# Performance work log

Hardware: AMD Instinct MI355X
Metric: run time of the kernel (lower is better)

## Reference

```python
import math
import jax, jax.numpy as jnp
import numpy as np

TEMPERATURE = 1.0
TARGET_VARIANCE = 2.0


def _l2_normalize(x, eps=1e-12):
    # matches F.normalize(dim=-1): x / max(||x||_2, eps)
    n = jnp.linalg.norm(x, axis=-1, keepdims=True)
    return x / jnp.maximum(n, eps)


def setup_inputs() -> dict:
    key = jax.random.key(0)
    k1, k2, k3 = jax.random.split(key, 3)
    B, L, D = 16, 2048, 512
    embs = jax.random.normal(k1, (B, L, D), dtype=jnp.float32)
    clip_embs = jax.random.normal(k2, (B, L, D), dtype=jnp.float32)
    mask = jax.random.randint(k3, (B, L), 0, 2, dtype=jnp.int32)
    return {"embs": embs, "clip_embs": clip_embs, "mask": mask}


def reference(embs, clip_embs, mask):
    B, L, D = embs.shape
    p = _l2_normalize(embs)
    q = _l2_normalize(clip_embs)

    # m_b = number of valid tokens per sample; original slices the first m rows
    m = jnp.sum(mask > 0, axis=-1)                      # [B]
    valid = jnp.arange(L)[None, :] < m[:, None]         # [B, L]
    colm = valid[:, None, :]                            # [B, 1, L] column mask

    # batched p @ q^T over the full padded length, masked afterwards
    logits = jnp.einsum('bid,bjd->bij', p, q) / TEMPERATURE  # [B, L, L]
    neg = jnp.finfo(logits.dtype).min
    logp = jax.nn.log_softmax(jnp.where(colm, logits, neg), axis=-1)

    # Gaussian distance weights: base_weight[i, j] = |i - j|
    idx = jnp.arange(L)
    dist = jnp.abs(idx[:, None] - idx[None, :]).astype(embs.dtype)  # [L, L]
    t_un = jnp.exp(-(dist ** 2) / (2.0 * TARGET_VARIANCE ** 2)) / TARGET_VARIANCE * math.sqrt(math.pi * 2.0)
    target = jax.nn.softmax(jnp.where(colm, t_un[None], neg), axis=-1)  # [B, L, L]

    # KL(target || softmax(logits)) = target * (log target - logp), summed over cols
    safe_t = jnp.where(colm, target, 1.0)
    kl = jnp.where(colm, target * (jnp.log(safe_t) - logp), 0.0)
    row_sum = jnp.sum(kl, axis=-1)                      # [B, L]

    # mean over the m valid rows, then mean over batch
    per_sample = jnp.sum(jnp.where(valid, row_sum, 0.0), axis=-1) / m.astype(embs.dtype)
    return jnp.sum(per_sample) / B
```

## Files before the change

### kernel.cpp

```cpp
#include <hip/hip_runtime.h>
#include <hip/hip_bf16.h>

#define BB 16
#define LL 2048
#define DD 512
#define BL (BB*LL)
#define RADIUS 15
#define CF 1.25331414f
#define NSL 6
#define NII 16

typedef __attribute__((ext_vector_type(8))) short short8_t;
typedef __attribute__((ext_vector_type(4))) float f32x4;
typedef __attribute__((ext_vector_type(2))) long long2_t;

static __device__ __forceinline__ unsigned short f2bf(float x){
  unsigned int u = __float_as_uint(x);
  return (unsigned short)((u + 0x7fffu + ((u >> 16) & 1u)) >> 16);
}

static __device__ __forceinline__ void gld_lds16(const void* g, void* l){
  __builtin_amdgcn_global_load_lds(
      (const __attribute__((address_space(1))) unsigned int*)g,
      (__attribute__((address_space(3))) unsigned int*)l, 16, 0, 0);
}

#if __has_builtin(__builtin_amdgcn_cvt_pk_fp8_f32)
static __device__ __forceinline__ long f2fp8x8(float4 x0, float4 x1){
  int w0 = __builtin_amdgcn_cvt_pk_fp8_f32(x0.x, x0.y, 0, false);
  w0     = __builtin_amdgcn_cvt_pk_fp8_f32(x0.z, x0.w, w0, true);
  int w1 = __builtin_amdgcn_cvt_pk_fp8_f32(x1.x, x1.y, 0, false);
  w1     = __builtin_amdgcn_cvt_pk_fp8_f32(x1.z, x1.w, w1, true);
  return ((long)(unsigned)w1 << 32) | (unsigned)w0;
}
#else
static __device__ __forceinline__ unsigned f2fp8_1(float xf){
  unsigned x = __float_as_uint(xf);
  unsigned s = (x >> 24) & 0x80u;
  unsigned ax = x & 0x7fffffffu;
  if (ax >= 0x43e80000u) return s | 0x7eu;
  if (ax <  0x3a800000u) return s;
  unsigned exp = ax >> 23;
  if (exp <= 120){
    unsigned man = (ax & 0x7fffffu) | 0x800000u;
    int rsh = 141 - (int)exp;
    unsigned keep = man >> rsh;
    unsigned rem  = man & ((1u << rsh) - 1u);
    unsigned half = 1u << (rsh - 1);
    keep += (rem > half || (rem == half && (keep & 1u)));
    return s | keep;
  }
  unsigned keep = ax >> 20;
  unsigned rem  = ax & 0xfffffu;
  keep += (rem > 0x80000u || (rem == 0x80000u && (keep & 1u)));
  int code = (int)keep - (120 << 3);
  if (code >= 0x7f) code = 0x7e;
  return s | (unsigned)code;
}
static __device__ __forceinline__ long f2fp8x8(float4 x0, float4 x1){
  unsigned long o = 0;
  o |= (unsigned long)f2fp8_1(x0.x);
  o |= (unsigned long)f2fp8_1(x0.y) << 8;
  o |= (unsigned long)f2fp8_1(x0.z) << 16;
  o |= (unsigned long)f2fp8_1(x0.w) << 24;
  o |= (unsigned long)f2fp8_1(x1.x) << 32;
  o |= (unsigned long)f2fp8_1(x1.y) << 40;
  o |= (unsigned long)f2fp8_1(x1.z) << 48;
  o |= (unsigned long)f2fp8_1(x1.w) << 56;
  return (long)o;
}
#endif


__global__ void mcount_kernel(const int* __restrict__ mask, int* __restrict__ mout){
  int b = blockIdx.x;
  int s = 0;
  for (int j = threadIdx.x; j < LL; j += 256) s += (mask[(size_t)b*LL + j] > 0) ? 1 : 0;
  __shared__ int sred[256];
  sred[threadIdx.x] = s; __syncthreads();
  for (int k = 128; k; k >>= 1){
    if (threadIdx.x < k) sred[threadIdx.x] += sred[threadIdx.x + k];
    __syncthreads();
  }
  if (threadIdx.x == 0) mout[b] = sred[0];
}

__global__ __launch_bounds__(256) void precvt(const float* __restrict__ embs,
                                              const float* __restrict__ clip,
                                              const int* __restrict__ mcnt,
                                              unsigned char* __restrict__ p8,
                                              unsigned char* __restrict__ q8){
  const int lane = threadIdx.x & 63;
  const int g    = lane >> 4;
  const int c    = lane & 15;
  const int base = blockIdx.x * 16 + (threadIdx.x >> 6) * 4;
  const int gw   = base + g;

  const float* src; unsigned char* dst; int r, b; bool isP;
  if (gw < BL){ isP = true;  b = gw >> 11; r = gw & 2047;
                src = embs + (size_t)gw * DD; dst = p8 + (size_t)b * LL * DD; }
  else        { isP = false; int g2 = gw - BL; b = g2 >> 11; r = g2 & 2047;
                src = clip + (size_t)g2 * DD; dst = q8 + (size_t)b * LL * DD; }
  const int M   = mcnt[b];
  const int RND = isP ? ((M + 127) & ~127) : ((M + 15) & ~15);
  if (r >= RND) return;

  float4 v[8];
  #pragma unroll
  for (int k = 0; k < 8; ++k) v[k] = *(const float4*)(src + c * 32 + k * 4);
  float ss = 0.f;
  #pragma unroll
  for (int k = 0; k < 8; ++k)
    ss += v[k].x*v[k].x + v[k].y*v[k].y + v[k].z*v[k].z + v[k].w*v[k].w;
  #pragma unroll
  for (int m = 1; m < 16; m <<= 1) ss += __shfl_xor(ss, m, 64);
  const float s = 1.0f / fmaxf(sqrtf(ss), 1e-12f);
  #pragma unroll
  for (int k = 0; k < 8; ++k){
    v[k].x *= s; v[k].y *= s; v[k].z *= s; v[k].w *= s;
  }
  const long o0 = f2fp8x8(v[0], v[1]);
  const long o1 = f2fp8x8(v[2], v[3]);
  const long o2 = f2fp8x8(v[4], v[5]);
  const long o3 = f2fp8x8(v[6], v[7]);
  const int xr = (r >> 2) & 3;
  long2_t lo, hi;
  switch (xr){
    case 0: lo = (long2_t){o0, o1}; hi = (long2_t){o2, o3}; break;
    case 1: lo = (long2_t){o1, o0}; hi = (long2_t){o3, o2}; break;
    case 2: lo = (long2_t){o2, o3}; hi = (long2_t){o0, o1}; break;
    default:lo = (long2_t){o3, o2}; hi = (long2_t){o1, o0}; break;
  }
  unsigned char* wb = dst + ((size_t)(c * LL + r) << 5);
  *(long2_t*)(wb)      = lo;
  *(long2_t*)(wb + 16) = hi;
}

__global__ __launch_bounds__(256, 4) void gram8(
    const unsigned char* __restrict__ p8, const unsigned char* __restrict__ q8,
    const int* __restrict__ mcnt, float* __restrict__ part )
{
  const int bid = blockIdx.x;
  const int xcd = bid & 7;
  const int b   = (xcd << 1) | ((bid >> 3) & 1);
  const int ii  = (bid >> 4) & (NII - 1);
  const int js  = bid >> 8;
  const int M   = mcnt[b];
  const int nIt = (M + 127) >> 7;
  if (ii >= nIt) return;

  __shared__ alignas(16) unsigned char bsm[3][8192];
  __shared__ float gt[RADIUS + 1];

  const int tid  = threadIdx.x;
  const int wave = tid >> 6;
  const int lane = tid & 63;
  const int col  = lane & 15;
  const int kg   = lane >> 4;
  const int kswz = (kg ^ (col >> 2)) << 3;

  if (tid <= RADIUS)
    gt[tid] = expm1f(CF * __expf(-(float)(tid * tid) * 0.125f));
  __syncthreads();

  const unsigned char* pb = p8 + (size_t)b * LL * DD;
  const unsigned char* qb = q8 + (size_t)b * LL * DD;
  const int njt = (M + 15) >> 4;
  const int S   = (njt > js) ? ((njt - js + NSL - 1) / NSL) : 0;
  if (S == 0) return;

  #define STAGE(BF, JT) do {                                                     \
    const int _j0 = (JT) << 4;                                                   \
    _Pragma("unroll")                                                            \
    for (int u = 0; u < 2; ++u){                                                 \
      const int _kb0 = (wave << 1) + (u << 3);                                   \
      gld_lds16(qb + ((size_t)((_kb0 + (lane >> 5)) * LL + _j0) << 5)            \
                   + ((lane & 31) << 4),                                         \
                (void*)&bsm[BF][_kb0 << 9]);                                     \
    }                                                                            \
  } while (0)

  const int iw = (ii << 7) + (wave << 5);

  long a0[16], a1[16];
  #pragma unroll
  for (int kb = 0; kb < 16; ++kb){
    a0[kb] = *(const long*)(pb + ((size_t)(kb * LL + iw      + col) << 5) + kswz);
    a1[kb] = *(const long*)(pb + ((size_t)(kb * LL + iw + 16 + col) << 5) + kswz);
  }
  #pragma unroll
  for (int kb = 0; kb < 16; ++kb){
    asm volatile("" : "+v"(a0[kb]));
    asm volatile("" : "+v"(a1[kb]));
  }

  float es0[4]={0,0,0,0}, ls0[4]={0,0,0,0}, bg0[4]={0,0,0,0};
  float es1[4]={0,0,0,0}, ls1[4]={0,0,0,0}, bg1[4]={0,0,0,0};

  STAGE(0, js);
  if (S > 1) STAGE(1, js + NSL);

  for (int s = 0; s < S; ++s){
    if (s + 1 < S) { asm volatile("s_waitcnt vmcnt(2)" ::: "memory"); }
    else           { asm volatile("s_waitcnt vmcnt(0)" ::: "memory"); }
    __builtin_amdgcn_s_barrier();
    __builtin_amdgcn_sched_barrier(0);
    if (s + 2 < S) STAGE((s + 2) % 3, js + NSL * (s + 2));

    const int j0 = (js + NSL * s) << 4;
    f32x4 c0 = {0.f,0.f,0.f,0.f}, c1 = {0.f,0.f,0.f,0.f};
    const unsigned char* lb = &bsm[s % 3][(col << 5) + kswz];
    __builtin_amdgcn_s_setprio(1);
    #pragma unroll
    for (int kb = 0; kb < 16; ++kb){
      long bf8 = *(const long*)(lb + (kb << 9));
      c0 = __builtin_amdgcn_mfma_f32_16x16x32_fp8_fp8(a0[kb], bf8, c0, 0, 0, 0);
      c1 = __builtin_amdgcn_mfma_f32_16x16x32_fp8_fp8(a1[kb], bf8, c1, 0, 0, 0);
    }
    __builtin_amdgcn_s_setprio(0);
    const int j = j0 + col;
    if (j < M){
      const int dt0 = j - iw - (kg << 2);
      #pragma unroll
      for (int r = 0; r < 4; ++r){
        float lg = c0[r];
        es0[r] += __expf(lg); ls0[r] += lg;
        int d = dt0 - r; int ad = d < 0 ? -d : d;
        if (ad <= RADIUS) bg0[r] += gt[ad] * lg;
        float lh = c1[r];
        es1[r] += __expf(lh); ls1[r] += lh;
        int d1 = dt0 - 16 - r; int ad1 = d1 < 0 ? -d1 : d1;
        if (ad1 <= RADIUS) bg1[r] += gt[ad1] * lh;
      }
    }
  }
  #undef STAGE

  #pragma unroll
  for (int m = 1; m < 16; m <<= 1){
    #pragma unroll
    for (int r = 0; r < 4; ++r){
      es0[r] += __shfl_xor(es0[r], m, 64); es1[r] += __shfl_xor(es1[r], m, 64);
      ls0[r] += __shfl_xor(ls0[r], m, 64); ls1[r] += __shfl_xor(ls1[r], m, 64);
      bg0[r] += __shfl_xor(bg0[r], m, 64); bg1[r] += __shfl_xor(bg1[r], m, 64);
    }
  }
  if (col == 0){
    #pragma unroll
    for (int r = 0; r < 4; ++r){
      int ia = iw + (kg << 2) + r;
      *(float4*)&part[(((size_t)b * LL + ia) * NSL + js) * 4] = make_float4(es0[r], ls0[r], bg0[r], 0.f);
      int ib = ia + 16;
      *(float4*)&part[(((size_t)b * LL + ib) * NSL + js) * 4] = make_float4(es1[r], ls1[r], bg1[r], 0.f);
    }
  }
}

__global__ __launch_bounds__(256) void finalize1(const float* __restrict__ part,
                                                 const int* __restrict__ mcnt,
                                                 float* __restrict__ psum){
  const int b = blockIdx.x;
  const int M = mcnt[b];
  __shared__ float e1s[16], tts[16], S1[16], TT[16], red[256];
  const int tid = threadIdx.x;
  if (tid < 16){
    float u  = CF * __expf(-(float)(tid * tid) * 0.125f);
    float eu = __expf(u);
    e1s[tid] = eu - 1.0f;
    tts[tid] = u * eu;
  }
  __syncthreads();
  if (tid == 0){
    float a = 0.f, c = 0.f;
    S1[0] = 0.f; TT[0] = 0.f;
    for (int d = 1; d <= RADIUS; ++d){ a += e1s[d]; c += tts[d]; S1[d] = a; TT[d] = c; }
  }
  __syncthreads();
  const float e10 = e1s[0], tt0 = tts[0];
  float acc = 0.f;
  for (int i = tid; i < M; i += 256){
    float es = 0.f, ls = 0.f, bg = 0.f;
    #pragma unroll
    for (int h = 0; h < NSL; ++h){
      float4 v = *(const float4*)&part[(((size_t)b * LL + i) * NSL + h) * 4];
      es += v.x; ls += v.y; bg += v.z;
    }
    int rl = i < RADIUS ? i : RADIUS;
    int rr = (M - 1 - i) < RADIUS ? (M - 1 - i) : RADIUS;
    float Zt = (float)M + e10 + S1[rl] + S1[rr];
    float U  = tt0 + TT[rl] + TT[rr];
    acc += (U - ls - bg) / Zt + logf(es) - logf(Zt);
  }
  red[tid] = acc; __syncthreads();
  for (int k = 128; k; k >>= 1){
    if (tid < k) red[tid] += red[tid + k];
    __syncthreads();
  }
  if (tid == 0) psum[b] = red[0] / (float)M;
}

__global__ void finalize2(const float* __restrict__ psum, float* __restrict__ out){
  if (threadIdx.x == 0){
    float a = 0.f;
    for (int b = 0; b < BB; ++b) a += psum[b];
    out[0] = a / (float)BB;
  }
}

#define TI 32
#define TJ 32
#define LSTR 520

__global__ void fb_qnorm(const float* __restrict__ clip, float* __restrict__ invq){
  int row = blockIdx.x;
  const float* p = clip + (size_t)row * DD;
  float4 v = *(const float4*)(p + (threadIdx.x << 2));
  float ss = v.x*v.x + v.y*v.y + v.z*v.z + v.w*v.w;
  for (int m = 32; m; m >>= 1) ss += __shfl_down(ss, m, 64);
  __shared__ float red[2];
  if ((threadIdx.x & 63) == 0) red[threadIdx.x >> 6] = ss;
  __syncthreads();
  if (threadIdx.x == 0)
    invq[row] = 1.0f / fmaxf(sqrtf(red[0] + red[1]), 1e-12f);
}

__global__ __launch_bounds__(256) void fb_main(
    const float* __restrict__ embs, const float* __restrict__ clip,
    const float* __restrict__ invq, const int* __restrict__ mcnt,
    float* __restrict__ row_sums)
{
  const int b  = blockIdx.y;
  const int M  = mcnt[b];
  const int i0 = blockIdx.x * TI;
  if (i0 >= M) return;
  __shared__ alignas(16) unsigned short qlds[TJ * LSTR];
  __shared__ float gtab[RADIUS + 1];
  __shared__ float partials[2][TI][3];
  const int tid  = threadIdx.x;
  const int wave = tid >> 6;
  const int lane = tid & 63;
  const int col  = lane & 15;
  const int kg   = lane >> 4;
  const int isub = wave >> 1;
  const int jsub = wave & 1;
  const int iw   = i0 + isub * 16;
  if (tid <= RADIUS)
    gtab[tid] = expm1f(CF * expf(-(float)(tid * tid) * 0.125f));
  const int arow = iw + col;
  const float* prow = embs + ((size_t)b * LL + arow) * DD;
  float ss = 0.f;
  for (int kb = 0; kb < 16; ++kb){
    float4 x0 = *(const float4*)(prow + kb * 32 + kg * 8);
    float4 x1 = *(const float4*)(prow + kb * 32 + kg * 8 + 4);
    ss += x0.x*x0.x + x0.y*x0.y + x0.z*x0.z + x0.w*x0.w
        + x1.x*x1.x + x1.y*x1.y + x1.z*x1.z + x1.w*x1.w;
  }
  ss += __shfl_xor(ss, 16, 64);
  ss += __shfl_xor(ss, 32, 64);
  const float sp = 1.0f / fmaxf(sqrtf(ss), 1e-12f);
  short8_t afrag[16];
  for (int kb = 0; kb < 16; ++kb){
    float4 x0 = *(const float4*)(prow + kb * 32 + kg * 8);
    float4 x1 = *(const float4*)(prow + kb * 32 + kg * 8 + 4);
    short8_t f;
    f[0]=(short)f2bf(x0.x*sp); f[1]=(short)f2bf(x0.y*sp);
    f[2]=(short)f2bf(x0.z*sp); f[3]=(short)f2bf(x0.w*sp);
    f[4]=(short)f2bf(x1.x*sp); f[5]=(short)f2bf(x1.y*sp);
    f[6]=(short)f2bf(x1.z*sp); f[7]=(short)f2bf(x1.w*sp);
    afrag[kb] = f;
  }
  float es[4]={0,0,0,0}, lsm[4]={0,0,0,0}, bg[4]={0,0,0,0};
  const int nj = (M + TJ - 1) / TJ;
  for (int jt = 0; jt < nj; ++jt){
    const int jb = jt * TJ;
    __syncthreads();
    {
      const float* qbase = clip + ((size_t)b * LL + jb) * DD;
      for (int u = 0; u < 16; ++u){
        int f  = u * 256 + tid;
        int r  = f >> 7, c4 = f & 127;
        int j  = jb + r;
        ushort4 wv = make_ushort4(0,0,0,0);
        if (j < M){
          float s = invq[b * LL + j];
          float4 x = *(const float4*)(qbase + ((size_t)r << 9) + (c4 << 2));
          wv = make_ushort4(f2bf(x.x*s), f2bf(x.y*s), f2bf(x.z*s), f2bf(x.w*s));
        }
        *reinterpret_cast<ushort4*>(&qlds[r * LSTR + (c4 << 2)]) = wv;
      }
    }
    __syncthreads();
    const int j0 = jb + jsub * 16;
    f32x4 acc = {0.f,0.f,0.f,0.f};
    const unsigned short* bbase = &qlds[(jsub * 16 + col) * LSTR + kg * 8];
    #pragma unroll
    for (int kb = 0; kb < 16; ++kb){
      short8_t bfrag = *reinterpret_cast<const short8_t*>(bbase + kb * 32);
      acc = __builtin_amdgcn_mfma_f32_16x16x32_bf16(afrag[kb], bfrag, acc, 0, 0, 0);
    }
    const int j = j0 + col;
    if (j < M){
      const int dt = j - iw - kg * 4;
      #pragma unroll
      for (int r = 0; r < 4; ++r){
        float lg = acc[r];
        es[r]  += expf(lg);
        lsm[r] += lg;
        int d = dt - r; int ad = d < 0 ? -d : d;
        if (ad <= RADIUS) bg[r] += gtab[ad] * lg;
      }
    }
  }
  #pragma unroll
  for (int m = 1; m < 16; m <<= 1){
    #pragma unroll
    for (int r = 0; r < 4; ++r){
      es[r]  += __shfl_xor(es[r],  m, 64);
      lsm[r] += __shfl_xor(lsm[r], m, 64);
      bg[r]  += __shfl_xor(bg[r],  m, 64);
    }
  }
  if (col == 0){
    #pragma unroll
    for (int r = 0; r < 4; ++r){
      int lrow = isub * 16 + kg * 4 + r;
      partials[jsub][lrow][0] = es[r];
      partials[jsub][lrow][1] = lsm[r];
      partials[jsub][lrow][2] = bg[r];
    }
  }
  __syncthreads();
  if (tid < TI){
    int i = i0 + tid;
    if (i < M){
      float esf = partials[0][tid][0] + partials[1][tid][0];
      float lsf = partials[0][tid][1] + partials[1][tid][1];
      float bgf = partials[0][tid][2] + partials[1][tid][2];
      int dlo = (-RADIUS < -i) ? -i : -RADIUS;
      int dhi = (RADIUS > M - 1 - i) ? (M - 1 - i) : RADIUS;
      float Zt = (float)M, U = 0.f;
      for (int d = dlo; d <= dhi; ++d){
        float uu = CF * expf(-(float)(d * d) * 0.125f);
        float eu = expf(uu);
        Zt += eu - 1.0f;
        U  += uu * eu;
      }
      row_sums[(size_t)b * LL + i] = (U - lsf - bgf) / Zt + logf(esf / Zt);
    }
  }
}

__global__ void fb_finalize(const float* __restrict__ row_sums,
                            const int* __restrict__ mcnt, float* __restrict__ out){
  __shared__ float red[256];
  float acc = 0.f;
  for (int b = 0; b < BB; ++b){
    int M = mcnt[b];
    float s = 0.f;
    for (int i = threadIdx.x; i < M; i += 256) s += row_sums[(size_t)b * LL + i];
    red[threadIdx.x] = s; __syncthreads();
    for (int k = 128; k; k >>= 1){
      if (threadIdx.x < k) red[threadIdx.x] += red[threadIdx.x + k];
      __syncthreads();
    }
    if (threadIdx.x == 0) acc += red[0] / (float)M;
    __syncthreads();
  }
  if (threadIdx.x == 0) out[0] = acc / (float)BB;
}


extern "C" void kernel_launch(void* const* d_in, const int* in_sizes, int n_in,
                              void* d_out, int out_size, void* d_ws, size_t ws_size,
                              hipStream_t stream) {
  const float* embs = (const float*)d_in[0];
  const float* clip = (const float*)d_in[1];
  const int*   mask = (const int*)d_in[2];
  float* out = (float*)d_out;

  const size_t REQ = (size_t)2 * BL * DD
                   + (size_t)BB * LL * NSL * 4 * sizeof(float)
                   + 64 * sizeof(float);
  if (ws_size >= REQ){
    unsigned char* p8 = (unsigned char*)d_ws;
    unsigned char* q8 = p8 + (size_t)BL * DD;
    float* part = (float*)(q8 + (size_t)BL * DD);
    float* psum = part + (size_t)BB * LL * NSL * 4;
    int*   mcnt = (int*)(psum + 16);

    mcount_kernel<<<dim3(BB), 256, 0, stream>>>(mask, mcnt);
    precvt<<<dim3(2 * BL / 16), 256, 0, stream>>>(embs, clip, mcnt, p8, q8);
    gram8<<<dim3(16 * NSL * NII), 256, 0, stream>>>(p8, q8, mcnt, part);
    finalize1<<<dim3(BB), 256, 0, stream>>>(part, mcnt, psum);
    finalize2<<<1, 64, 0, stream>>>(psum, out);
  } else {
    float* ws   = (float*)d_ws;
    float* invq = ws;
    int*   mcnt = (int*)(ws + BL);
    float* rows = ws + BL + 16;
    fb_qnorm<<<dim3(BL), 128, 0, stream>>>(clip, invq);
    mcount_kernel<<<dim3(BB), 256, 0, stream>>>(mask, mcnt);
    fb_main<<<dim3(LL / TI, BB), 256, 0, stream>>>(embs, clip, invq, mcnt, rows);
    fb_finalize<<<1, 256, 0, stream>>>(rows, mcnt, out);
  }
}
```

Before: 55.65 us.

## Widen gram tile to 32 columns with double-buffered LDS staging

Doubles the column tile per loop iteration from 16 to 32, so each LDS stage holds 16KB and feeds four MFMA chains. This reuses the register-resident A fragments twice as much per stage and halves the number of loop iterations and barriers. It switches from a three-stage to a two-stage LDS pipeline that waits for all loads each iteration. It also skips the band-weight math on tiles far from the diagonal and lowers the occupancy hint, which risks exposing load latency and adding register pressure.

```diff
diff --git a/kernel.cpp b/kernel.cpp
--- a/kernel.cpp
+++ b/kernel.cpp
@@ -102,7 +102,7 @@
   else        { isP = false; int g2 = gw - BL; b = g2 >> 11; r = g2 & 2047;
                 src = clip + (size_t)g2 * DD; dst = q8 + (size_t)b * LL * DD; }
   const int M   = mcnt[b];
-  const int RND = isP ? ((M + 127) & ~127) : ((M + 15) & ~15);
+  const int RND = isP ? ((M + 127) & ~127) : ((M + 31) & ~31);
   if (r >= RND) return;
 
   float4 v[8];
@@ -136,7 +136,7 @@
   *(long2_t*)(wb + 16) = hi;
 }
 
-__global__ __launch_bounds__(256, 4) void gram8(
+__global__ __launch_bounds__(256, 3) void gram10(
     const unsigned char* __restrict__ p8, const unsigned char* __restrict__ q8,
     const int* __restrict__ mcnt, float* __restrict__ part )
 {
@@ -149,7 +149,7 @@
   const int nIt = (M + 127) >> 7;
   if (ii >= nIt) return;
 
-  __shared__ alignas(16) unsigned char bsm[3][8192];
+  __shared__ alignas(16) unsigned char bsm[2][16384];
   __shared__ float gt[RADIUS + 1];
 
   const int tid  = threadIdx.x;
@@ -165,18 +165,17 @@
 
   const unsigned char* pb = p8 + (size_t)b * LL * DD;
   const unsigned char* qb = q8 + (size_t)b * LL * DD;
-  const int njt = (M + 15) >> 4;
+  const int njt = (M + 31) >> 5;
   const int S   = (njt > js) ? ((njt - js + NSL - 1) / NSL) : 0;
   if (S == 0) return;
 
   #define STAGE(BF, JT) do {                                                     \
-    const int _j0 = (JT) << 4;                                                   \
+    const int _j0 = (JT) << 5;                                                   \
     _Pragma("unroll")                                                            \
-    for (int u = 0; u < 2; ++u){                                                 \
-      const int _kb0 = (wave << 1) + (u << 3);                                   \
-      gld_lds16(qb + ((size_t)((_kb0 + (lane >> 5)) * LL + _j0) << 5)            \
-                   + ((lane & 31) << 4),                                         \
-                (void*)&bsm[BF][_kb0 << 9]);                                     \
+    for (int u = 0; u < 4; ++u){                                                 \
+      const int _kb = (wave << 2) + u;                                           \
+      gld_lds16(qb + ((size_t)(_kb * LL + _j0) << 5) + (lane << 4),              \
+                (void*)&bsm[BF][_kb << 10]);                                     \
     }                                                                            \
   } while (0)
 
@@ -188,51 +187,70 @@
     a0[kb] = *(const long*)(pb + ((size_t)(kb * LL + iw      + col) << 5) + kswz);
     a1[kb] = *(const long*)(pb + ((size_t)(kb * LL + iw + 16 + col) << 5) + kswz);
   }
-  #pragma unroll
-  for (int kb = 0; kb < 16; ++kb){
-    asm volatile("" : "+v"(a0[kb]));
-    asm volatile("" : "+v"(a1[kb]));
-  }
 
   float es0[4]={0,0,0,0}, ls0[4]={0,0,0,0}, bg0[4]={0,0,0,0};
   float es1[4]={0,0,0,0}, ls1[4]={0,0,0,0}, bg1[4]={0,0,0,0};
 
   STAGE(0, js);
-  if (S > 1) STAGE(1, js + NSL);
-
+  asm volatile("s_waitcnt vmcnt(0)" ::: "memory");
+  __builtin_amdgcn_s_barrier();
+  __builtin_amdgcn_sched_barrier(0);
+
+  int buf = 0;
   for (int s = 0; s < S; ++s){
-    if (s + 1 < S) { asm volatile("s_waitcnt vmcnt(2)" ::: "memory"); }
-    else           { asm volatile("s_waitcnt vmcnt(0)" ::: "memory"); }
+    if (s + 1 < S) STAGE(buf ^ 1, js + NSL * (s + 1));
+
+    const int j0 = (js + NSL * s) << 5;
+    f32x4 cA0 = {0.f,0.f,0.f,0.f}, cA1 = {0.f,0.f,0.f,0.f};
+    f32x4 cB0 = {0.f,0.f,0.f,0.f}, cB1 = {0.f,0.f,0.f,0.f};
+    const unsigned char* lb = &bsm[buf][(col << 5) + kswz];
+    #pragma unroll
+    for (int kb = 0; kb < 16; ++kb){
+      long bfA = *(const long*)(lb + (kb << 10));
+      long bfB = *(const long*)(lb + (kb << 10) + 512);
+      cA0 = __builtin_amdgcn_mfma_f32_16x16x32_fp8_fp8(a0[kb], bfA, cA0, 0, 0, 0);
+      cA1 = __builtin_amdgcn_mfma_f32_16x16x32_fp8_fp8(a1[kb], bfA, cA1, 0, 0, 0);
+      cB0 = __builtin_amdgcn_mfma_f32_16x16x32_fp8_fp8(a0[kb], bfB, cB0, 0, 0, 0);
+      cB1 = __builtin_amdgcn_mfma_f32_16x16x32_fp8_fp8(a1[kb], bfB, cB1, 0, 0, 0);
+    }
+    const int jA = j0 + col, jB = j0 + 16 + col;
+    const bool bandw = (j0 + 31 >= iw - RADIUS) && (j0 <= iw + 31 + RADIUS);
+    const int dtA = jA - iw - (kg << 2);
+    if (jA < M){
+      #pragma unroll
+      for (int r = 0; r < 4; ++r){
+        float lg = cA0[r];
+        float lh = cA1[r];
+        es0[r] += __expf(lg); ls0[r] += lg;
+        es1[r] += __expf(lh); ls1[r] += lh;
+        if (bandw){
+          int d = dtA - r; int ad = d < 0 ? -d : d;
+          if (ad <= RADIUS) bg0[r] += gt[ad] * lg;
+          int d1 = dtA - 16 - r; int ad1 = d1 < 0 ? -d1 : d1;
+          if (ad1 <= RADIUS) bg1[r] += gt[ad1] * lh;
+        }
+      }
+    }
+    if (jB < M){
+      const int dtB = dtA + 16;
+      #pragma unroll
+      for (int r = 0; r < 4; ++r){
+        float lg = cB0[r];
+        float lh = cB1[r];
+        es0[r] += __expf(lg); ls0[r] += lg;
+        es1[r] += __expf(lh); ls1[r] += lh;
+        if (bandw){
+          int d = dtB - r; int ad = d < 0 ? -d : d;
+          if (ad <= RADIUS) bg0[r] += gt[ad] * lg;
+          int d1 = dtB - 16 - r; int ad1 = d1 < 0 ? -d1 : d1;
+          if (ad1 <= RADIUS) bg1[r] += gt[ad1] * lh;
+        }
+      }
+    }
+    asm volatile("s_waitcnt vmcnt(0)" ::: "memory");
     __builtin_amdgcn_s_barrier();
     __builtin_amdgcn_sched_barrier(0);
-    if (s + 2 < S) STAGE((s + 2) % 3, js + NSL * (s + 2));
-
-    const int j0 = (js + NSL * s) << 4;
-    f32x4 c0 = {0.f,0.f,0.f,0.f}, c1 = {0.f,0.f,0.f,0.f};
-    const unsigned char* lb = &bsm[s % 3][(col << 5) + kswz];
-    __builtin_amdgcn_s_setprio(1);
-    #pragma unroll
-    for (int kb = 0; kb < 16; ++kb){
-      long bf8 = *(const long*)(lb + (kb << 9));
-      c0 = __builtin_amdgcn_mfma_f32_16x16x32_fp8_fp8(a0[kb], bf8, c0, 0, 0, 0);
-      c1 = __builtin_amdgcn_mfma_f32_16x16x32_fp8_fp8(a1[kb], bf8, c1, 0, 0, 0);
-    }
-    __builtin_amdgcn_s_setprio(0);
-    const int j = j0 + col;
-    if (j < M){
-      const int dt0 = j - iw - (kg << 2);
-      #pragma unroll
-      for (int r = 0; r < 4; ++r){
-        float lg = c0[r];
-        es0[r] += __expf(lg); ls0[r] += lg;
-        int d = dt0 - r; int ad = d < 0 ? -d : d;
-        if (ad <= RADIUS) bg0[r] += gt[ad] * lg;
-        float lh = c1[r];
-        es1[r] += __expf(lh); ls1[r] += lh;
-        int d1 = dt0 - 16 - r; int ad1 = d1 < 0 ? -d1 : d1;
-        if (ad1 <= RADIUS) bg1[r] += gt[ad1] * lh;
-      }
-    }
+    buf ^= 1;
   }
   #undef STAGE
 
@@ -490,7 +508,7 @@
 
     mcount_kernel<<<dim3(BB), 256, 0, stream>>>(mask, mcnt);
     precvt<<<dim3(2 * BL / 16), 256, 0, stream>>>(embs, clip, mcnt, p8, q8);
-    gram8<<<dim3(16 * NSL * NII), 256, 0, stream>>>(p8, q8, mcnt, part);
+    gram10<<<dim3(16 * NSL * NII), 256, 0, stream>>>(p8, q8, mcnt, part);
     finalize1<<<dim3(BB), 256, 0, stream>>>(part, mcnt, psum);
     finalize2<<<1, 64, 0, stream>>>(psum, out);
   } else {
```

After: 58.31 us. +4.8%, slower.

## Halve per-wave row tile in gram kernel and raise grid and occupancy

Applied to the files above, without the earlier changes.

The gram kernel now gives each wave 16 query rows (64 per block) instead of 32 (128 per block). It doubles the row-block count to 32, cuts the column slices from 6 to 5, and raises the launch bound to 6 blocks per CU. This lowers register pressure and adds parallelism and occupancy, but each staged key tile is reused by half as many MFMAs, so LDS and global traffic per FLOP rises. The setprio hints around the MFMA loop are also removed.

```diff
diff --git a/kernel.cpp b/kernel.cpp
--- a/kernel.cpp
+++ b/kernel.cpp
@@ -7,8 +7,8 @@
 #define BL (BB*LL)
 #define RADIUS 15
 #define CF 1.25331414f
-#define NSL 6
-#define NII 16
+#define NSL 5
+#define NII 32
 
 typedef __attribute__((ext_vector_type(8))) short short8_t;
 typedef __attribute__((ext_vector_type(4))) float f32x4;
@@ -136,7 +136,7 @@
   *(long2_t*)(wb + 16) = hi;
 }
 
-__global__ __launch_bounds__(256, 4) void gram8(
+__global__ __launch_bounds__(256, 6) void gram12(
     const unsigned char* __restrict__ p8, const unsigned char* __restrict__ q8,
     const int* __restrict__ mcnt, float* __restrict__ part )
 {
@@ -144,9 +144,9 @@
   const int xcd = bid & 7;
   const int b   = (xcd << 1) | ((bid >> 3) & 1);
   const int ii  = (bid >> 4) & (NII - 1);
-  const int js  = bid >> 8;
+  const int js  = bid >> 9;
   const int M   = mcnt[b];
-  const int nIt = (M + 127) >> 7;
+  const int nIt = (M + 63) >> 6;
   if (ii >= nIt) return;
 
   __shared__ alignas(16) unsigned char bsm[3][8192];
@@ -180,22 +180,16 @@
     }                                                                            \
   } while (0)
 
-  const int iw = (ii << 7) + (wave << 5);
-
-  long a0[16], a1[16];
-  #pragma unroll
-  for (int kb = 0; kb < 16; ++kb){
-    a0[kb] = *(const long*)(pb + ((size_t)(kb * LL + iw      + col) << 5) + kswz);
-    a1[kb] = *(const long*)(pb + ((size_t)(kb * LL + iw + 16 + col) << 5) + kswz);
-  }
-  #pragma unroll
-  for (int kb = 0; kb < 16; ++kb){
-    asm volatile("" : "+v"(a0[kb]));
-    asm volatile("" : "+v"(a1[kb]));
-  }
+  const int iw = (ii << 6) + (wave << 4);
+
+  long a0[16];
+  #pragma unroll
+  for (int kb = 0; kb < 16; ++kb)
+    a0[kb] = *(const long*)(pb + ((size_t)(kb * LL + iw + col) << 5) + kswz);
+  #pragma unroll
+  for (int kb = 0; kb < 16; ++kb) asm volatile("" : "+v"(a0[kb]));
 
   float es0[4]={0,0,0,0}, ls0[4]={0,0,0,0}, bg0[4]={0,0,0,0};
-  float es1[4]={0,0,0,0}, ls1[4]={0,0,0,0}, bg1[4]={0,0,0,0};
 
   STAGE(0, js);
   if (S > 1) STAGE(1, js + NSL);
@@ -208,16 +202,13 @@
     if (s + 2 < S) STAGE((s + 2) % 3, js + NSL * (s + 2));
 
     const int j0 = (js + NSL * s) << 4;
-    f32x4 c0 = {0.f,0.f,0.f,0.f}, c1 = {0.f,0.f,0.f,0.f};
+    f32x4 c0 = {0.f,0.f,0.f,0.f};
     const unsigned char* lb = &bsm[s % 3][(col << 5) + kswz];
-    __builtin_amdgcn_s_setprio(1);
     #pragma unroll
     for (int kb = 0; kb < 16; ++kb){
       long bf8 = *(const long*)(lb + (kb << 9));
       c0 = __builtin_amdgcn_mfma_f32_16x16x32_fp8_fp8(a0[kb], bf8, c0, 0, 0, 0);
-      c1 = __builtin_amdgcn_mfma_f32_16x16x32_fp8_fp8(a1[kb], bf8, c1, 0, 0, 0);
-    }
-    __builtin_amdgcn_s_setprio(0);
+    }
     const int j = j0 + col;
     if (j < M){
       const int dt0 = j - iw - (kg << 2);
@@ -227,10 +218,6 @@
         es0[r] += __expf(lg); ls0[r] += lg;
         int d = dt0 - r; int ad = d < 0 ? -d : d;
         if (ad <= RADIUS) bg0[r] += gt[ad] * lg;
-        float lh = c1[r];
-        es1[r] += __expf(lh); ls1[r] += lh;
-        int d1 = dt0 - 16 - r; int ad1 = d1 < 0 ? -d1 : d1;
-        if (ad1 <= RADIUS) bg1[r] += gt[ad1] * lh;
       }
     }
   }
@@ -240,18 +227,17 @@
   for (int m = 1; m < 16; m <<= 1){
     #pragma unroll
     for (int r = 0; r < 4; ++r){
-      es0[r] += __shfl_xor(es0[r], m, 64); es1[r] += __shfl_xor(es1[r], m, 64);
-      ls0[r] += __shfl_xor(ls0[r], m, 64); ls1[r] += __shfl_xor(ls1[r], m, 64);
-      bg0[r] += __shfl_xor(bg0[r], m, 64); bg1[r] += __shfl_xor(bg1[r], m, 64);
+      es0[r] += __shfl_xor(es0[r], m, 64);
+      ls0[r] += __shfl_xor(ls0[r], m, 64);
+      bg0[r] += __shfl_xor(bg0[r], m, 64);
     }
   }
   if (col == 0){
     #pragma unroll
     for (int r = 0; r < 4; ++r){
       int ia = iw + (kg << 2) + r;
-      *(float4*)&part[(((size_t)b * LL + ia) * NSL + js) * 4] = make_float4(es0[r], ls0[r], bg0[r], 0.f);
-      int ib = ia + 16;
-      *(float4*)&part[(((size_t)b * LL + ib) * NSL + js) * 4] = make_float4(es1[r], ls1[r], bg1[r], 0.f);
+      *(float4*)&part[(((size_t)b * LL + ia) * NSL + js) * 4] =
+          make_float4(es0[r], ls0[r], bg0[r], 0.f);
     }
   }
 }
@@ -490,7 +476,7 @@
 
     mcount_kernel<<<dim3(BB), 256, 0, stream>>>(mask, mcnt);
     precvt<<<dim3(2 * BL / 16), 256, 0, stream>>>(embs, clip, mcnt, p8, q8);
-    gram8<<<dim3(16 * NSL * NII), 256, 0, stream>>>(p8, q8, mcnt, part);
+    gram12<<<dim3(16 * NSL * NII), 256, 0, stream>>>(p8, q8, mcnt, part);
     finalize1<<<dim3(BB), 256, 0, stream>>>(part, mcnt, psum);
     finalize2<<<1, 64, 0, stream>>>(psum, out);
   } else {
```

After: 53.93 us. -3.1%, faster.
